# Performance work log

Hardware: AMD Instinct MI355X
Metric: run time of the kernel (lower is better)

Reference implementation:

```python
import jax, jax.numpy as jnp
import numpy as np

N, E, H = 50000, 800000, 4
IN_C, HID, OUT = 256, 64, 64
NEG_SLOPE = 0.2   # PyG GATConv default leaky_relu slope
EPS_BN = 1e-5
EPS_SM = 1e-16    # PyG softmax denominator eps


def setup_inputs() -> dict:
    key = jax.random.key(0)
    ks = jax.random.split(key, 16)
    inp = {
        "x": jax.random.normal(ks[0], (N, IN_C), jnp.float32),
        "edge_index": jax.random.randint(ks[1], (2, E), 0, N, jnp.int32),
    }
    dims = [(IN_C, HID), (HID, HID), (HID, OUT)]
    j = 2
    for l, (di, do) in enumerate(dims):
        s = 1.0 / np.sqrt(di)
        inp[f"W{l}"] = jax.random.normal(ks[j], (di, H * do), jnp.float32) * s; j += 1
        inp[f"as{l}"] = jax.random.normal(ks[j], (H, do), jnp.float32) * 0.1; j += 1
        inp[f"ad{l}"] = jax.random.normal(ks[j], (H, do), jnp.float32) * 0.1; j += 1
        inp[f"b{l}"] = jnp.zeros((do,), jnp.float32)
    for l in range(2):  # BN after all but the last conv
        inp[f"g{l}"] = jnp.ones((HID,), jnp.float32)
        inp[f"be{l}"] = jnp.zeros((HID,), jnp.float32)
    return inp


def _gat_layer(x, src, dst, W, a_src, a_dst, bias):
    """PyG GATConv, heads=H, concat=False (mean over heads), add_self_loops already in src/dst."""
    n = x.shape[0]
    C = a_src.shape[1]
    h = (x @ W).reshape(n, H, C)                      # [N,H,C]
    a_l = jnp.einsum('nhc,hc->nh', h, a_src)          # src attention term per node
    a_r = jnp.einsum('nhc,hc->nh', h, a_dst)          # dst attention term per node
    e = jax.nn.leaky_relu(a_l[src] + a_r[dst], NEG_SLOPE)   # [E',H]
    # segment softmax over incoming edges of each dst node
    m = jax.ops.segment_max(e, dst, num_segments=n)
    m = jnp.where(jnp.isfinite(m), m, 0.0)
    p = jnp.exp(e - m[dst])
    den = jax.ops.segment_sum(p, dst, num_segments=n)
    alpha = p / (den[dst] + EPS_SM)                   # [E',H]
    msg = h[src] * alpha[:, :, None]                  # [E',H,C]
    out = jax.ops.segment_sum(msg, dst, num_segments=n)
    return out.mean(axis=1) + bias                    # concat=False -> head mean, then bias


def _bn(x, g, b):
    # BatchNorm1d training-mode statistics (biased variance), eps=1e-5
    mu = x.mean(axis=0)
    var = x.var(axis=0)
    return (x - mu) * jax.lax.rsqrt(var + EPS_BN) * g + b


def reference(x, edge_index, W0, as0, ad0, b0, W1, as1, ad1, b1,
              W2, as2, ad2, b2, g0, be0, g1, be1):
    n = x.shape[0]
    loops = jnp.arange(n, dtype=edge_index.dtype)
    src = jnp.concatenate([edge_index[0], loops])
    dst = jnp.concatenate([edge_index[1], loops])

    h = _gat_layer(x, src, dst, W0, as0, ad0, b0)
    h = jax.nn.relu(_bn(h, g0, be0))                  # dropout: eval mode (identity)
    h = _gat_layer(h, src, dst, W1, as1, ad1, b1)
    h = jax.nn.relu(_bn(h, g1, be1))
    out = _gat_layer(h, src, dst, W2, as2, ad2, b2)
    return out
```

## Files before the change

### kernel.cpp

```cpp
#include <hip/hip_runtime.h>
#include <hip/hip_fp16.h>
#include <math.h>

constexpr float NEG_SLOPE = 0.2f;
constexpr float EPS_BN = 1e-5f;
constexpr float EPS_SM = 1e-16f;

typedef _Float16 half8 __attribute__((ext_vector_type(8)));
typedef _Float16 half4v __attribute__((ext_vector_type(4)));
typedef float f32x4 __attribute__((ext_vector_type(4)));

__device__ __forceinline__ float lrelu(float x){ return x >= 0.f ? x : NEG_SLOPE * x; }

__global__ void k_init(int* cnt, int n, float* bn, int* tick){
  int i = blockIdx.x * blockDim.x + threadIdx.x;
  if (i < n) cnt[i] = 0;
  if (i < 256) bn[i] = 0.f;
  if (i < 4) tick[i] = 0;
}

__global__ void k_x2h(const float* __restrict__ x, _Float16* __restrict__ xh, int total4){
  int t = blockIdx.x * blockDim.x + threadIdx.x;
  if (t >= total4) return;
  float4 v = ((const float4*)x)[t];
  half4v h = {(_Float16)v.x, (_Float16)v.y, (_Float16)v.z, (_Float16)v.w};
  *(half4v*)(xh + (size_t)t * 4) = h;
}

__global__ void k_convW(const float* __restrict__ W, _Float16* __restrict__ Wt, int K){
  int t = blockIdx.x * blockDim.x + threadIdx.x;
  if (t >= K * 256) return;
  int n = t & 255, k = t >> 8;
  Wt[(size_t)n * K + k] = (_Float16)W[(size_t)k * 256 + n];
}

__global__ void k_count(const int* __restrict__ ei, int E, int N, int* __restrict__ cnt){
  int e = blockIdx.x * blockDim.x + threadIdx.x;
  if (e >= E + N) return;
  int dst = (e < E) ? ei[E + e] : (e - E);
  atomicAdd(&cnt[dst], 1);
}

__global__ __launch_bounds__(256) void k_blocksum(const int* __restrict__ cnt, int n, int chunk,
                                                  int* __restrict__ part){
  __shared__ int s[256];
  int b = blockIdx.x, t = threadIdx.x;
  int lo = b * chunk, hi = min(n, lo + chunk);
  int v = 0;
  for (int i = lo + t; i < hi; i += 256) v += cnt[i];
  s[t] = v;
  __syncthreads();
  #pragma unroll
  for (int off = 128; off > 0; off >>= 1){
    if (t < off) s[t] += s[t + off];
    __syncthreads();
  }
  if (t == 0) part[b] = s[0];
}

__global__ __launch_bounds__(256) void k_scanpart(int* __restrict__ part, int* __restrict__ ptr, int n){
  __shared__ int s[256];
  int t = threadIdx.x;
  int v = part[t];
  s[t] = v;
  __syncthreads();
  #pragma unroll
  for (int off = 1; off < 256; off <<= 1){
    int u = (t >= off) ? s[t - off] : 0;
    __syncthreads();
    s[t] += u;
    __syncthreads();
  }
  part[t] = s[t] - v;
  if (t == 255) ptr[n] = s[255];
}

__global__ __launch_bounds__(256) void k_localscan(const int* __restrict__ cnt, const int* __restrict__ part,
                                                   int n, int chunk, int* __restrict__ ptr,
                                                   int* __restrict__ cursor){
  __shared__ int s[256];
  int b = blockIdx.x, t = threadIdx.x;
  int i = b * chunk + t;
  int v = (t < chunk && i < n) ? cnt[i] : 0;
  s[t] = v;
  __syncthreads();
  #pragma unroll
  for (int off = 1; off < 256; off <<= 1){
    int u = (t >= off) ? s[t - off] : 0;
    __syncthreads();
    s[t] += u;
    __syncthreads();
  }
  if (t < chunk && i < n){
    int ex = part[b] + s[t] - v;
    ptr[i] = ex;
    cursor[i] = ex;
  }
}

__global__ void k_fill(const int* __restrict__ ei, int E, int N,
                       int* __restrict__ cursor, int* __restrict__ csr_src){
  int e = blockIdx.x * blockDim.x + threadIdx.x;
  if (e >= E + N) return;
  int src, dst;
  if (e < E){ src = ei[e]; dst = ei[E + e]; } else { src = e - E; dst = e - E; }
  int slot = atomicAdd(&cursor[dst], 1);
  csr_src[slot] = src;
}

__global__ __launch_bounds__(256) void k_gemm(const _Float16* __restrict__ Xh,
    const _Float16* __restrict__ Wt, const float* __restrict__ a_s, const float* __restrict__ a_d,
    __half* __restrict__ hb, float* __restrict__ al, float* __restrict__ ar, int nrows, int K){
  __shared__ _Float16 Alds[4][128][8];
  __shared__ _Float16 Blds[4][64][8];
  int tid = threadIdx.x;
  int m0 = blockIdx.x * 128;
  int head = blockIdx.y;
  int n0 = head * 64;
  int w = tid >> 6, l = tid & 63;
  int lm = l & 15, lq = l >> 4;
  int qs = tid & 3, rs = tid >> 2;
  f32x4 acc[2][4] = {};

  for (int k0 = 0; k0 < K; k0 += 32){
    #pragma unroll
    for (int it = 0; it < 2; it++){
      int row = it * 64 + rs;
      int gr = m0 + row;
      half8 v = {};
      if (gr < nrows) v = *(const half8*)(Xh + (size_t)gr * K + k0 + qs * 8);
      *(half8*)&Alds[qs][row][0] = v;
    }
    *(half8*)&Blds[qs][rs][0] = *(const half8*)(Wt + (size_t)(n0 + rs) * K + k0 + qs * 8);
    __syncthreads();
    half8 af0 = *(const half8*)&Alds[lq][w * 32 + lm][0];
    half8 af1 = *(const half8*)&Alds[lq][w * 32 + 16 + lm][0];
    #pragma unroll
    for (int nt = 0; nt < 4; nt++){
      half8 bf = *(const half8*)&Blds[lq][nt * 16 + lm][0];
      acc[0][nt] = __builtin_amdgcn_mfma_f32_16x16x32_f16(af0, bf, acc[0][nt], 0, 0, 0);
      acc[1][nt] = __builtin_amdgcn_mfma_f32_16x16x32_f16(af1, bf, acc[1][nt], 0, 0, 0);
    }
    __syncthreads();
  }

  float asv[4], adv[4];
  #pragma unroll
  for (int nt = 0; nt < 4; nt++){
    asv[nt] = a_s[n0 + nt * 16 + lm];
    adv[nt] = a_d[n0 + nt * 16 + lm];
  }
  #pragma unroll
  for (int s = 0; s < 2; s++){
    #pragma unroll
    for (int reg = 0; reg < 4; reg++){
      float sl = 0.f, sr = 0.f;
      #pragma unroll
      for (int nt = 0; nt < 4; nt++){
        sl += acc[s][nt][reg] * asv[nt];
        sr += acc[s][nt][reg] * adv[nt];
      }
      #pragma unroll
      for (int off = 1; off < 16; off <<= 1){
        sl += __shfl_xor(sl, off);
        sr += __shfl_xor(sr, off);
      }
      int grow = m0 + w * 32 + s * 16 + lq * 4 + reg;
      if (lm == 0 && grow < nrows){
        al[(size_t)grow * 4 + head] = sl;
        ar[(size_t)grow * 4 + head] = sr;
      }
    }
  }
  #pragma unroll
  for (int s = 0; s < 2; s++){
    #pragma unroll
    for (int nt = 0; nt < 4; nt++){
      #pragma unroll
      for (int reg = 0; reg < 4; reg++){
        int grow = m0 + w * 32 + s * 16 + lq * 4 + reg;
        if (grow < nrows)
          hb[(size_t)grow * 256 + n0 + nt * 16 + lm] = __float2half(acc[s][nt][reg]);
      }
    }
  }
}

__global__ __launch_bounds__(256) void k_node(const int* __restrict__ ptr,
    const int* __restrict__ csr, const __half* __restrict__ hb,
    const float* __restrict__ al, const float* __restrict__ ar,
    const float* __restrict__ bias, float* __restrict__ out, int N){
  __shared__ float4 wsm[4][64];
  __shared__ int    ssm[4][64];
  int n = (blockIdx.x * blockDim.x + threadIdx.x) >> 6;
  int lane = threadIdx.x & 63;
  int wv = threadIdx.x >> 6;
  if (n >= N) return;
  int beg = ptr[n], end = ptr[n + 1];
  int deg = end - beg;
  float4 arv = *(const float4*)(ar + (size_t)n * 4);
  int hd = lane >> 4;
  int cg = (lane & 15) * 4;
  float ax = 0.f, ay = 0.f, az = 0.f, aw = 0.f;

  if (deg <= 64){
    int idx = beg + lane;
    bool act = idx < end;
    int mye = act ? csr[idx] : 0;
    float e0 = -1e30f, e1 = -1e30f, e2 = -1e30f, e3 = -1e30f;
    if (act){
      float4 av = *(const float4*)(al + (size_t)mye * 4);
      e0 = lrelu(av.x + arv.x); e1 = lrelu(av.y + arv.y);
      e2 = lrelu(av.z + arv.z); e3 = lrelu(av.w + arv.w);
    }
    float m0 = e0, m1 = e1, m2 = e2, m3 = e3;
    #pragma unroll
    for (int off = 32; off > 0; off >>= 1){
      m0 = fmaxf(m0, __shfl_xor(m0, off));
      m1 = fmaxf(m1, __shfl_xor(m1, off));
      m2 = fmaxf(m2, __shfl_xor(m2, off));
      m3 = fmaxf(m3, __shfl_xor(m3, off));
    }
    float w0 = __expf(e0 - m0), w1 = __expf(e1 - m1);
    float w2 = __expf(e2 - m2), w3 = __expf(e3 - m3);
    float d0 = w0, d1 = w1, d2 = w2, d3 = w3;
    #pragma unroll
    for (int off = 32; off > 0; off >>= 1){
      d0 += __shfl_xor(d0, off);
      d1 += __shfl_xor(d1, off);
      d2 += __shfl_xor(d2, off);
      d3 += __shfl_xor(d3, off);
    }
    wsm[wv][lane] = make_float4(w0 / (d0 + EPS_SM), w1 / (d1 + EPS_SM),
                                w2 / (d2 + EPS_SM), w3 / (d3 + EPS_SM));
    ssm[wv][lane] = mye;
    __builtin_amdgcn_wave_barrier();
    const float* wbase = (const float*)&wsm[wv][0];
    #pragma unroll 2
    for (int j = 0; j < deg; j++){
      int s = ssm[wv][j];
      float w = wbase[j * 4 + hd];
      ushort4 u = *(const ushort4*)(hb + (size_t)s * 256 + hd * 64 + cg);
      ax += __half2float(__ushort_as_half(u.x)) * w;
      ay += __half2float(__ushort_as_half(u.y)) * w;
      az += __half2float(__ushort_as_half(u.z)) * w;
      aw += __half2float(__ushort_as_half(u.w)) * w;
    }
  } else {
    float m0 = -1e30f, m1 = -1e30f, m2 = -1e30f, m3 = -1e30f;
    for (int i = beg + lane; i < end; i += 64){
      int s = csr[i];
      float4 av = *(const float4*)(al + (size_t)s * 4);
      m0 = fmaxf(m0, lrelu(av.x + arv.x));
      m1 = fmaxf(m1, lrelu(av.y + arv.y));
      m2 = fmaxf(m2, lrelu(av.z + arv.z));
      m3 = fmaxf(m3, lrelu(av.w + arv.w));
    }
    #pragma unroll
    for (int off = 32; off > 0; off >>= 1){
      m0 = fmaxf(m0, __shfl_xor(m0, off));
      m1 = fmaxf(m1, __shfl_xor(m1, off));
      m2 = fmaxf(m2, __shfl_xor(m2, off));
      m3 = fmaxf(m3, __shfl_xor(m3, off));
    }
    float d0 = 0.f, d1 = 0.f, d2 = 0.f, d3 = 0.f;
    for (int i = beg + lane; i < end; i += 64){
      int s = csr[i];
      float4 av = *(const float4*)(al + (size_t)s * 4);
      d0 += __expf(lrelu(av.x + arv.x) - m0);
      d1 += __expf(lrelu(av.y + arv.y) - m1);
      d2 += __expf(lrelu(av.z + arv.z) - m2);
      d3 += __expf(lrelu(av.w + arv.w) - m3);
    }
    #pragma unroll
    for (int off = 32; off > 0; off >>= 1){
      d0 += __shfl_xor(d0, off);
      d1 += __shfl_xor(d1, off);
      d2 += __shfl_xor(d2, off);
      d3 += __shfl_xor(d3, off);
    }
    float i0 = 1.f / (d0 + EPS_SM), i1 = 1.f / (d1 + EPS_SM);
    float i2 = 1.f / (d2 + EPS_SM), i3 = 1.f / (d3 + EPS_SM);
    float arh = hd == 0 ? arv.x : hd == 1 ? arv.y : hd == 2 ? arv.z : arv.w;
    float mh  = hd == 0 ? m0 : hd == 1 ? m1 : hd == 2 ? m2 : m3;
    float ih  = hd == 0 ? i0 : hd == 1 ? i1 : hd == 2 ? i2 : i3;
    for (int i = beg; i < end; i++){
      int s = csr[i];
      float w = __expf(lrelu(al[(size_t)s * 4 + hd] + arh) - mh) * ih;
      ushort4 u = *(const ushort4*)(hb + (size_t)s * 256 + hd * 64 + cg);
      ax += __half2float(__ushort_as_half(u.x)) * w;
      ay += __half2float(__ushort_as_half(u.y)) * w;
      az += __half2float(__ushort_as_half(u.z)) * w;
      aw += __half2float(__ushort_as_half(u.w)) * w;
    }
  }

  #pragma unroll
  for (int off = 16; off <= 32; off <<= 1){
    ax += __shfl_xor(ax, off);
    ay += __shfl_xor(ay, off);
    az += __shfl_xor(az, off);
    aw += __shfl_xor(aw, off);
  }
  if (lane < 16){
    float4 b4 = *(const float4*)(bias + cg);
    *(float4*)(out + (size_t)n * 64 + cg) =
        make_float4(ax * 0.25f + b4.x, ay * 0.25f + b4.y, az * 0.25f + b4.z, aw * 0.25f + b4.w);
  }
}

__global__ __launch_bounds__(256) void k_bnstats(const float* __restrict__ x, int N,
                                                 float* __restrict__ gsum, float* __restrict__ gsq,
                                                 int* __restrict__ tick,
                                                 float* __restrict__ mu, float* __restrict__ rstd){
  int c = threadIdx.x & 63;
  int rg = threadIdx.x >> 6;
  float s = 0.f, q = 0.f;
  for (int r = blockIdx.x * 4 + rg; r < N; r += gridDim.x * 4){
    float v = x[(size_t)r * 64 + c];
    s += v; q += v * v;
  }
  __shared__ float ls[4][64], lq[4][64];
  __shared__ int amLast;
  ls[rg][c] = s; lq[rg][c] = q;
  __syncthreads();
  if (rg == 0){
    s = ls[0][c] + ls[1][c] + ls[2][c] + ls[3][c];
    q = lq[0][c] + lq[1][c] + lq[2][c] + lq[3][c];
    atomicAdd(&gsum[c], s);
    atomicAdd(&gsq[c], q);
  }
  __threadfence();
  if (threadIdx.x == 0)
    amLast = (atomicAdd(tick, 1) == (int)gridDim.x - 1) ? 1 : 0;
  __syncthreads();
  if (amLast && threadIdx.x < 64){
    float gs = atomicAdd(&gsum[c], 0.f);
    float gq = atomicAdd(&gsq[c], 0.f);
    float m = gs / (float)N;
    float v = gq / (float)N - m * m;
    mu[c] = m;
    rstd[c] = rsqrtf(v + EPS_BN);
  }
}

__global__ void k_bnapply(const float* __restrict__ x, const float* __restrict__ mu,
                          const float* __restrict__ rstd, const float* __restrict__ g,
                          const float* __restrict__ be, _Float16* __restrict__ y, int total){
  int i = blockIdx.x * blockDim.x + threadIdx.x;
  if (i >= total) return;
  int c = i & 63;
  float v = (x[i] - mu[c]) * rstd[c] * g[c] + be[c];
  y[i] = (_Float16)fmaxf(v, 0.f);
}

extern "C" void kernel_launch(void* const* d_in, const int* in_sizes, int n_in,
                              void* d_out, int out_size, void* d_ws, size_t ws_size,
                              hipStream_t stream){
  const float* x  = (const float*)d_in[0];
  const int*   ei = (const int*)d_in[1];
  const float* W[3]  = {(const float*)d_in[2], (const float*)d_in[6],  (const float*)d_in[10]};
  const float* AS[3] = {(const float*)d_in[3], (const float*)d_in[7],  (const float*)d_in[11]};
  const float* AD[3] = {(const float*)d_in[4], (const float*)d_in[8],  (const float*)d_in[12]};
  const float* BI[3] = {(const float*)d_in[5], (const float*)d_in[9],  (const float*)d_in[13]};
  const float* G[2]  = {(const float*)d_in[14], (const float*)d_in[16]};
  const float* BE[2] = {(const float*)d_in[15], (const float*)d_in[17]};
  const int N = in_sizes[0] / 256;
  const int E = in_sizes[1] / 2;
  const int EN = E + N;

  char* wsb = (char*)d_ws;
  size_t off = 0;
  auto alloc = [&](size_t bytes) -> char* {
    char* p = wsb + off;
    off = (off + bytes + 255) & ~(size_t)255;
    return p;
  };
  int* cnt      = (int*)alloc((size_t)N * 4);
  int* cursor   = (int*)alloc((size_t)N * 4);
  int* rowptr   = (int*)alloc((size_t)(N + 1) * 4);
  int* part     = (int*)alloc(256 * 4);
  int* csr      = (int*)alloc((size_t)EN * 4);
  _Float16* xh0 = (_Float16*)alloc((size_t)N * 256 * 2);
  _Float16* Wt  = (_Float16*)alloc((size_t)256 * 256 * 2);
  __half* hb    = (__half*)alloc((size_t)N * 256 * 2);
  float* al     = (float*)alloc((size_t)N * 4 * 4);
  float* ar     = (float*)alloc((size_t)N * 4 * 4);
  float* bufA   = (float*)alloc((size_t)N * 64 * 4);
  _Float16* bufH= (_Float16*)alloc((size_t)N * 64 * 2);
  float* bn     = (float*)alloc(256 * 4);
  int*   tick   = (int*)alloc(4 * 4);
  float* murs   = (float*)alloc(128 * 4);

  const int chunk = (N + 255) / 256;

  k_init<<<(N + 255) / 256, 256, 0, stream>>>(cnt, N, bn, tick);
  k_count<<<(EN + 255) / 256, 256, 0, stream>>>(ei, E, N, cnt);
  k_blocksum<<<256, 256, 0, stream>>>(cnt, N, chunk, part);
  k_scanpart<<<1, 256, 0, stream>>>(part, rowptr, N);
  k_localscan<<<256, 256, 0, stream>>>(cnt, part, N, chunk, rowptr, cursor);
  k_fill<<<(EN + 255) / 256, 256, 0, stream>>>(ei, E, N, cursor, csr);
  k_x2h<<<(N * 64 + 255) / 256, 256, 0, stream>>>(x, xh0, N * 64);

  const _Float16* lin = xh0;
  for (int l = 0; l < 3; l++){
    int K = (l == 0) ? 256 : 64;
    k_convW<<<(K * 256 + 255) / 256, 256, 0, stream>>>(W[l], Wt, K);
    dim3 gg((N + 127) / 128, 4);
    k_gemm<<<gg, 256, 0, stream>>>(lin, Wt, AS[l], AD[l], hb, al, ar, N, K);
    float* outp = (l == 2) ? (float*)d_out : bufA;
    k_node<<<(N + 3) / 4, 256, 0, stream>>>(rowptr, csr, hb, al, ar, BI[l], outp, N);
    if (l < 2){
      float* gsum = bn + l * 128;
      float* gsq  = gsum + 64;
      k_bnstats<<<128, 256, 0, stream>>>(bufA, N, gsum, gsq, tick + l, murs, murs + 64);
      k_bnapply<<<(N * 64 + 255) / 256, 256, 0, stream>>>(bufA, murs, murs + 64, G[l], BE[l], bufH, N * 64);
      lin = bufH;
    }
  }
}
```

Measured before the change: 570.4 us.

## Fuse fp32-to-fp16 conversion and BN+ReLU into GEMM A-load, batch weight conversion

Result: faster. 555.5 us (-2.6%).

```diff
diff --git a/kernel.cpp b/kernel.cpp
--- a/kernel.cpp
+++ b/kernel.cpp
@@ -7,7 +7,6 @@
 constexpr float EPS_SM = 1e-16f;
 
 typedef _Float16 half8 __attribute__((ext_vector_type(8)));
-typedef _Float16 half4v __attribute__((ext_vector_type(4)));
 typedef float f32x4 __attribute__((ext_vector_type(4)));
 
 __device__ __forceinline__ float lrelu(float x){ return x >= 0.f ? x : NEG_SLOPE * x; }
@@ -19,19 +18,20 @@
   if (i < 4) tick[i] = 0;
 }
 
-__global__ void k_x2h(const float* __restrict__ x, _Float16* __restrict__ xh, int total4){
+__global__ void k_convW3(const float* __restrict__ W0, const float* __restrict__ W1,
+                         const float* __restrict__ W2, _Float16* __restrict__ Wt0,
+                         _Float16* __restrict__ Wt1, _Float16* __restrict__ Wt2){
   int t = blockIdx.x * blockDim.x + threadIdx.x;
-  if (t >= total4) return;
-  float4 v = ((const float4*)x)[t];
-  half4v h = {(_Float16)v.x, (_Float16)v.y, (_Float16)v.z, (_Float16)v.w};
-  *(half4v*)(xh + (size_t)t * 4) = h;
-}
-
-__global__ void k_convW(const float* __restrict__ W, _Float16* __restrict__ Wt, int K){
-  int t = blockIdx.x * blockDim.x + threadIdx.x;
-  if (t >= K * 256) return;
-  int n = t & 255, k = t >> 8;
-  Wt[(size_t)n * K + k] = (_Float16)W[(size_t)k * 256 + n];
+  if (t < 65536){
+    int n = t & 255, k = t >> 8;
+    Wt0[(size_t)n * 256 + k] = (_Float16)W0[(size_t)k * 256 + n];
+  } else if (t < 81920){
+    int u = t - 65536; int n = u & 255, k = u >> 8;
+    Wt1[(size_t)n * 64 + k] = (_Float16)W1[(size_t)k * 256 + n];
+  } else if (t < 98304){
+    int u = t - 81920; int n = u & 255, k = u >> 8;
+    Wt2[(size_t)n * 64 + k] = (_Float16)W2[(size_t)k * 256 + n];
+  }
 }
 
 __global__ void k_count(const int* __restrict__ ei, int E, int N, int* __restrict__ cnt){
@@ -108,9 +108,10 @@
   csr_src[slot] = src;
 }
 
-__global__ __launch_bounds__(256) void k_gemm(const _Float16* __restrict__ Xh,
+__global__ __launch_bounds__(256) void k_gemm(const float* __restrict__ X,
     const _Float16* __restrict__ Wt, const float* __restrict__ a_s, const float* __restrict__ a_d,
-    __half* __restrict__ hb, float* __restrict__ al, float* __restrict__ ar, int nrows, int K){
+    __half* __restrict__ hb, float* __restrict__ al, float* __restrict__ ar, int nrows, int K,
+    const float* __restrict__ scale, const float* __restrict__ shift){
   __shared__ _Float16 Alds[4][128][8];
   __shared__ _Float16 Blds[4][64][8];
   int tid = threadIdx.x;
@@ -123,13 +124,35 @@
   f32x4 acc[2][4] = {};
 
   for (int k0 = 0; k0 < K; k0 += 32){
+    float4 sc0, sc1, sh0, sh1;
+    if (scale){
+      sc0 = *(const float4*)(scale + k0 + qs * 8);
+      sc1 = *(const float4*)(scale + k0 + qs * 8 + 4);
+      sh0 = *(const float4*)(shift + k0 + qs * 8);
+      sh1 = *(const float4*)(shift + k0 + qs * 8 + 4);
+    }
     #pragma unroll
     for (int it = 0; it < 2; it++){
       int row = it * 64 + rs;
       int gr = m0 + row;
-      half8 v = {};
-      if (gr < nrows) v = *(const half8*)(Xh + (size_t)gr * K + k0 + qs * 8);
-      *(half8*)&Alds[qs][row][0] = v;
+      float4 v0 = make_float4(0,0,0,0), v1 = make_float4(0,0,0,0);
+      if (gr < nrows){
+        v0 = *(const float4*)(X + (size_t)gr * K + k0 + qs * 8);
+        v1 = *(const float4*)(X + (size_t)gr * K + k0 + qs * 8 + 4);
+      }
+      if (scale){
+        v0.x = fmaxf(fmaf(v0.x, sc0.x, sh0.x), 0.f);
+        v0.y = fmaxf(fmaf(v0.y, sc0.y, sh0.y), 0.f);
+        v0.z = fmaxf(fmaf(v0.z, sc0.z, sh0.z), 0.f);
+        v0.w = fmaxf(fmaf(v0.w, sc0.w, sh0.w), 0.f);
+        v1.x = fmaxf(fmaf(v1.x, sc1.x, sh1.x), 0.f);
+        v1.y = fmaxf(fmaf(v1.y, sc1.y, sh1.y), 0.f);
+        v1.z = fmaxf(fmaf(v1.z, sc1.z, sh1.z), 0.f);
+        v1.w = fmaxf(fmaf(v1.w, sc1.w, sh1.w), 0.f);
+      }
+      half8 h = {(_Float16)v0.x, (_Float16)v0.y, (_Float16)v0.z, (_Float16)v0.w,
+                 (_Float16)v1.x, (_Float16)v1.y, (_Float16)v1.z, (_Float16)v1.w};
+      *(half8*)&Alds[qs][row][0] = h;
     }
     *(half8*)&Blds[qs][rs][0] = *(const half8*)(Wt + (size_t)(n0 + rs) * K + k0 + qs * 8);
     __syncthreads();
@@ -190,8 +213,7 @@
     const int* __restrict__ csr, const __half* __restrict__ hb,
     const float* __restrict__ al, const float* __restrict__ ar,
     const float* __restrict__ bias, float* __restrict__ out, int N){
-  __shared__ float4 wsm[4][64];
-  __shared__ int    ssm[4][64];
+  __shared__ int2 ssw[4][64][4];
   int n = (blockIdx.x * blockDim.x + threadIdx.x) >> 6;
   int lane = threadIdx.x & 63;
   int wv = threadIdx.x >> 6;
@@ -201,6 +223,7 @@
   float4 arv = *(const float4*)(ar + (size_t)n * 4);
   int hd = lane >> 4;
   int cg = (lane & 15) * 4;
+  const __half* hbase = hb + hd * 64 + cg;
   float ax = 0.f, ay = 0.f, az = 0.f, aw = 0.f;
 
   if (deg <= 64){
@@ -231,20 +254,22 @@
       d2 += __shfl_xor(d2, off);
       d3 += __shfl_xor(d3, off);
     }
-    wsm[wv][lane] = make_float4(w0 / (d0 + EPS_SM), w1 / (d1 + EPS_SM),
-                                w2 / (d2 + EPS_SM), w3 / (d3 + EPS_SM));
-    ssm[wv][lane] = mye;
+    int4* wr = (int4*)&ssw[wv][lane][0];
+    wr[0] = make_int4(mye, __float_as_int(w0 / (d0 + EPS_SM)),
+                      mye, __float_as_int(w1 / (d1 + EPS_SM)));
+    wr[1] = make_int4(mye, __float_as_int(w2 / (d2 + EPS_SM)),
+                      mye, __float_as_int(w3 / (d3 + EPS_SM)));
     __builtin_amdgcn_wave_barrier();
-    const float* wbase = (const float*)&wsm[wv][0];
-    #pragma unroll 2
+    const int2* phd = &ssw[wv][0][hd];
+    #pragma unroll 4
     for (int j = 0; j < deg; j++){
-      int s = ssm[wv][j];
-      float w = wbase[j * 4 + hd];
-      ushort4 u = *(const ushort4*)(hb + (size_t)s * 256 + hd * 64 + cg);
-      ax += __half2float(__ushort_as_half(u.x)) * w;
-      ay += __half2float(__ushort_as_half(u.y)) * w;
-      az += __half2float(__ushort_as_half(u.z)) * w;
-      aw += __half2float(__ushort_as_half(u.w)) * w;
+      int2 sw = phd[j * 4];
+      float w = __int_as_float(sw.y);
+      ushort4 u = *(const ushort4*)(hbase + (size_t)sw.x * 256);
+      ax = fmaf(__half2float(__ushort_as_half(u.x)), w, ax);
+      ay = fmaf(__half2float(__ushort_as_half(u.y)), w, ay);
+      az = fmaf(__half2float(__ushort_as_half(u.z)), w, az);
+      aw = fmaf(__half2float(__ushort_as_half(u.w)), w, aw);
     }
   } else {
     float m0 = -1e30f, m1 = -1e30f, m2 = -1e30f, m3 = -1e30f;
@@ -287,11 +312,11 @@
     for (int i = beg; i < end; i++){
       int s = csr[i];
       float w = __expf(lrelu(al[(size_t)s * 4 + hd] + arh) - mh) * ih;
-      ushort4 u = *(const ushort4*)(hb + (size_t)s * 256 + hd * 64 + cg);
-      ax += __half2float(__ushort_as_half(u.x)) * w;
-      ay += __half2float(__ushort_as_half(u.y)) * w;
-      az += __half2float(__ushort_as_half(u.z)) * w;
-      aw += __half2float(__ushort_as_half(u.w)) * w;
+      ushort4 u = *(const ushort4*)(hbase + (size_t)s * 256);
+      ax = fmaf(__half2float(__ushort_as_half(u.x)), w, ax);
+      ay = fmaf(__half2float(__ushort_as_half(u.y)), w, ay);
+      az = fmaf(__half2float(__ushort_as_half(u.z)), w, az);
+      aw = fmaf(__half2float(__ushort_as_half(u.w)), w, aw);
     }
   }
 
@@ -312,7 +337,8 @@
 __global__ __launch_bounds__(256) void k_bnstats(const float* __restrict__ x, int N,
                                                  float* __restrict__ gsum, float* __restrict__ gsq,
                                                  int* __restrict__ tick,
-                                                 float* __restrict__ mu, float* __restrict__ rstd){
+                                                 const float* __restrict__ g, const float* __restrict__ be,
+                                                 float* __restrict__ scale, float* __restrict__ shift){
   int c = threadIdx.x & 63;
   int rg = threadIdx.x >> 6;
   float s = 0.f, q = 0.f;
@@ -339,19 +365,10 @@
     float gq = atomicAdd(&gsq[c], 0.f);
     float m = gs / (float)N;
     float v = gq / (float)N - m * m;
-    mu[c] = m;
-    rstd[c] = rsqrtf(v + EPS_BN);
-  }
-}
-
-__global__ void k_bnapply(const float* __restrict__ x, const float* __restrict__ mu,
-                          const float* __restrict__ rstd, const float* __restrict__ g,
-                          const float* __restrict__ be, _Float16* __restrict__ y, int total){
-  int i = blockIdx.x * blockDim.x + threadIdx.x;
-  if (i >= total) return;
-  int c = i & 63;
-  float v = (x[i] - mu[c]) * rstd[c] * g[c] + be[c];
-  y[i] = (_Float16)fmaxf(v, 0.f);
+    float sc = g[c] * rsqrtf(v + EPS_BN);
+    scale[c] = sc;
+    shift[c] = be[c] - m * sc;
+  }
 }
 
 extern "C" void kernel_launch(void* const* d_in, const int* in_sizes, int n_in,
@@ -381,13 +398,13 @@
   int* rowptr   = (int*)alloc((size_t)(N + 1) * 4);
   int* part     = (int*)alloc(256 * 4);
   int* csr      = (int*)alloc((size_t)EN * 4);
-  _Float16* xh0 = (_Float16*)alloc((size_t)N * 256 * 2);
-  _Float16* Wt  = (_Float16*)alloc((size_t)256 * 256 * 2);
+  _Float16* Wt0 = (_Float16*)alloc((size_t)256 * 256 * 2);
+  _Float16* Wt1 = (_Float16*)alloc((size_t)64 * 256 * 2);
+  _Float16* Wt2 = (_Float16*)alloc((size_t)64 * 256 * 2);
   __half* hb    = (__half*)alloc((size_t)N * 256 * 2);
   float* al     = (float*)alloc((size_t)N * 4 * 4);
   float* ar     = (float*)alloc((size_t)N * 4 * 4);
   float* bufA   = (float*)alloc((size_t)N * 64 * 4);
-  _Float16* bufH= (_Float16*)alloc((size_t)N * 64 * 2);
   float* bn     = (float*)alloc(256 * 4);
   int*   tick   = (int*)alloc(4 * 4);
   float* murs   = (float*)alloc(128 * 4);
@@ -400,22 +417,23 @@
   k_scanpart<<<1, 256, 0, stream>>>(part, rowptr, N);
   k_localscan<<<256, 256, 0, stream>>>(cnt, part, N, chunk, rowptr, cursor);
   k_fill<<<(EN + 255) / 256, 256, 0, stream>>>(ei, E, N, cursor, csr);
-  k_x2h<<<(N * 64 + 255) / 256, 256, 0, stream>>>(x, xh0, N * 64);
-
-  const _Float16* lin = xh0;
+  k_convW3<<<384, 256, 0, stream>>>(W[0], W[1], W[2], Wt0, Wt1, Wt2);
+
+  const _Float16* Wt[3] = {Wt0, Wt1, Wt2};
+  const float* lin = x;
   for (int l = 0; l < 3; l++){
     int K = (l == 0) ? 256 : 64;
-    k_convW<<<(K * 256 + 255) / 256, 256, 0, stream>>>(W[l], Wt, K);
+    const float* sc = (l == 0) ? nullptr : murs;
+    const float* sh = (l == 0) ? nullptr : murs + 64;
     dim3 gg((N + 127) / 128, 4);
-    k_gemm<<<gg, 256, 0, stream>>>(lin, Wt, AS[l], AD[l], hb, al, ar, N, K);
+    k_gemm<<<gg, 256, 0, stream>>>(lin, Wt[l], AS[l], AD[l], hb, al, ar, N, K, sc, sh);
     float* outp = (l == 2) ? (float*)d_out : bufA;
     k_node<<<(N + 3) / 4, 256, 0, stream>>>(rowptr, csr, hb, al, ar, BI[l], outp, N);
     if (l < 2){
       float* gsum = bn + l * 128;
       float* gsq  = gsum + 64;
-      k_bnstats<<<128, 256, 0, stream>>>(bufA, N, gsum, gsq, tick + l, murs, murs + 64);
-      k_bnapply<<<(N * 64 + 255) / 256, 256, 0, stream>>>(bufA, murs, murs + 64, G[l], BE[l], bufH, N * 64);
-      lin = bufH;
-    }
-  }
-}
+      k_bnstats<<<128, 256, 0, stream>>>(bufA, N, gsum, gsq, tick + l, G[l], BE[l], murs, murs + 64);
+      lin = bufA;
+    }
+  }
+}
```
